# Kernel tuning notes

Measured on AMD Instinct MI355X. Metric: run time of the kernel, lower is better.

Reference implementation:

```python
import jax, jax.numpy as jnp
import numpy as np

N_NODES = 50000
N_EDGES = 800000
IN_DIM = 256     # state_size
HID = 256        # hidden_dim
ACT = 64         # action_size


def gcn_conv(x, src, dst, norm, W, b):
    # PyG GCNConv: out[dst] += norm_e * (x @ W)[src]; then + bias
    h = x @ W                               # [N, out]
    msg = h[src] * norm[:, None]            # [E+N, out]
    agg = jax.ops.segment_sum(msg, dst, num_segments=N_NODES)
    return agg + b


def gcn_norm(edge_index):
    # add self-loops, symmetric normalization deg^-1/2[src]*deg^-1/2[dst]
    loops = jnp.arange(N_NODES, dtype=edge_index.dtype)
    src = jnp.concatenate([edge_index[0], loops])
    dst = jnp.concatenate([edge_index[1], loops])
    deg = jax.ops.segment_sum(jnp.ones_like(dst, dtype=jnp.float32), dst,
                              num_segments=N_NODES)
    dinv = jnp.where(deg > 0, jax.lax.rsqrt(deg), 0.0)
    norm = dinv[src] * dinv[dst]            # [E+N]
    return src, dst, norm


def setup_inputs() -> dict:
    key = jax.random.key(0)
    ks = jax.random.split(key, 12)
    x = jax.random.normal(ks[0], (N_NODES, IN_DIM), dtype=jnp.float32)
    edge_index = jax.random.randint(ks[1], (2, N_EDGES), 0, N_NODES, dtype=jnp.int64)

    def glorot(k, shape):
        lim = float(np.sqrt(6.0 / (shape[0] + shape[1])))
        return jax.random.uniform(k, shape, jnp.float32, -lim, lim)

    return {
        "x": x, "edge_index": edge_index,
        "W1": glorot(ks[2], (IN_DIM, HID)), "b1": jnp.zeros((HID,), jnp.float32),
        "W2": glorot(ks[3], (HID, HID)),    "b2": jnp.zeros((HID,), jnp.float32),
        "fcW1": glorot(ks[4], (HID, HID)),  "fcb1": jnp.zeros((HID,), jnp.float32),
        "fcW2": glorot(ks[5], (HID, HID)),  "fcb2": jnp.zeros((HID,), jnp.float32),
        "fcW3": glorot(ks[6], (HID, ACT)),  "fcb3": jnp.zeros((ACT,), jnp.float32),
    }


def reference(x, edge_index, W1, b1, W2, b2, fcW1, fcb1, fcW2, fcb2, fcW3, fcb3):
    src, dst, norm = gcn_norm(edge_index)
    h = jax.nn.relu(gcn_conv(x, src, dst, norm, W1, b1))   # GNNLayer 1
    h = jax.nn.relu(gcn_conv(h, src, dst, norm, W2, b2))   # GNNLayer 2
    g = jax.nn.relu(jnp.mean(h, axis=0)[None, :])          # [1, HID]
    g = jax.nn.relu(g @ fcW1 + fcb1)
    g = jax.nn.relu(g @ fcW2 + fcb2)
    return g @ fcW3 + fcb3                                 # [1, ACT]
```

## Files before the change

kernel.cpp:

```cpp
#include <hip/hip_runtime.h>

#define N_NODES 50000
#define N_EDGES 800000
#define DIM 256
#define ACT 64
#define SCAN_B 256
#define SCAN_NB ((N_NODES + SCAN_B - 1) / SCAN_B)
#define SLICE_ELEMS ((size_t)N_NODES * 32)
#define AGG_CHUNKS 512
#define NPC ((N_NODES + AGG_CHUNKS - 1) / AGG_CHUNKS)
#define CSR_MAX (N_EDGES + 8 * N_NODES + 64)

typedef __attribute__((ext_vector_type(8))) short short8_t;
typedef __attribute__((ext_vector_type(4))) float f32x4;
typedef __attribute__((ext_vector_type(4))) unsigned short ushort4_t;

__device__ __forceinline__ unsigned short f2b(float x) {
    unsigned u = __float_as_uint(x);
    unsigned r = u + 0x7FFFu + ((u >> 16) & 1u);
    return (unsigned short)(r >> 16);
}


__global__ __launch_bounds__(256) void k_cvt_wt2(const float* __restrict__ W1,
                                                 const float* __restrict__ W2,
                                                 unsigned short* __restrict__ W1t,
                                                 unsigned short* __restrict__ W2t) {
    int b = blockIdx.x;
    const float* W = (b < 256) ? W1 : W2;
    unsigned short* Wt = (b < 256) ? W1t : W2t;
    int i = (b & 255) * 256 + threadIdx.x;
    int k = i >> 8, n = i & 255;
    Wt[n * DIM + k] = f2b(W[k * DIM + n]);
}


__global__ void k_deg_count(const int* __restrict__ ei, int* degi) {
    int e = blockIdx.x * blockDim.x + threadIdx.x;
    if (e < N_EDGES) atomicAdd(&degi[ei[N_EDGES + e]], 1);
}


__global__ __launch_bounds__(SCAN_B) void k_scan_local(const int* __restrict__ degi,
                                                       int* lexc, int* btot) {
    __shared__ int sm[SCAN_B];
    int t = threadIdx.x;
    int i = blockIdx.x * SCAN_B + t;
    int v = (i < N_NODES) ? ((degi[i] + 8) & ~7) : 0;
    sm[t] = v;
    __syncthreads();
#pragma unroll
    for (int off = 1; off < SCAN_B; off <<= 1) {
        int u = (t >= off) ? sm[t - off] : 0;
        __syncthreads();
        sm[t] += u;
        __syncthreads();
    }
    if (i < N_NODES) lexc[i] = sm[t] - v;
    if (t == SCAN_B - 1) btot[blockIdx.x] = sm[t];
}

__global__ __launch_bounds__(SCAN_B) void k_scan_tops(const int* __restrict__ btot,
                                                      int* bbase, int* rowstart) {
    __shared__ int sm[SCAN_B];
    int t = threadIdx.x;
    int v = (t < SCAN_NB) ? btot[t] : 0;
    sm[t] = v;
    __syncthreads();
#pragma unroll
    for (int off = 1; off < SCAN_B; off <<= 1) {
        int u = (t >= off) ? sm[t - off] : 0;
        __syncthreads();
        sm[t] += u;
        __syncthreads();
    }
    if (t < SCAN_NB) bbase[t] = sm[t] - v;
    if (t == SCAN_NB - 1) rowstart[N_NODES] = sm[t];
}

__global__ __launch_bounds__(SCAN_B) void k_scan_apply(const int* __restrict__ degi,
                                                       const int* __restrict__ lexc,
                                                       const int* __restrict__ bbase,
                                                       int* rowstart, int* fillpos,
                                                       float* dinv, unsigned* csr4) {
    int i = blockIdx.x * SCAN_B + threadIdx.x;
    if (i >= N_NODES) return;
    int rs = bbase[blockIdx.x] + lexc[i];
    rowstart[i] = rs;
    int d = degi[i] + 1;
    float di = rsqrtf((float)d);
    dinv[i] = di;
    csr4[rs] = ((unsigned)i << 16) | f2b(di * di);
    fillpos[i] = rs + 1;
}

__global__ void k_fill_edge(const int* __restrict__ ei,
                            const float* __restrict__ dinv, int* fillpos,
                            unsigned* csr4) {
    int e = blockIdx.x * blockDim.x + threadIdx.x;
    if (e < N_EDGES) {
        int s = ei[e];
        int d = ei[N_EDGES + e];
        int p = atomicAdd(&fillpos[d], 1);
        csr4[p] = ((unsigned)s << 16) | f2b(dinv[s] * dinv[d]);
    }
}


template <int AFP32>
__global__ __launch_bounds__(512) void k_gemm_mfma(const void* __restrict__ Ap,
                                                   const unsigned short* __restrict__ Wt,
                                                   unsigned short* __restrict__ H,
                                                   int M) {
    __shared__ char lds[49152];
    char* AsB = lds;
    char* BsB = lds + 16384;

    int tid = threadIdx.x;
    int w = tid >> 6;
    int l = tid & 63;
    int wr = w >> 2, wc = w & 3;
    int r0 = blockIdx.x * 128;

    f32x4 acc[4][4];
#pragma unroll
    for (int i = 0; i < 4; ++i)
#pragma unroll
        for (int j = 0; j < 4; ++j) acc[i][j] = (f32x4)(0.f);

    for (int kt = 0; kt < 4; ++kt) {
        int k0 = kt * 64;
#pragma unroll
        for (int i = 0; i < 2; ++i) {
            int c = tid + i * 512;
            int row = c >> 3, kc = c & 7;
            int gg = r0 + row; if (gg >= M) gg = M - 1;
            short8_t v;
            if (AFP32) {
                const float* A = (const float*)Ap;
                const float4* src = (const float4*)(A + (size_t)gg * DIM + k0 + kc * 8);
                float4 f0 = src[0], f1 = src[1];
                v[0] = (short)f2b(f0.x); v[1] = (short)f2b(f0.y);
                v[2] = (short)f2b(f0.z); v[3] = (short)f2b(f0.w);
                v[4] = (short)f2b(f1.x); v[5] = (short)f2b(f1.y);
                v[6] = (short)f2b(f1.z); v[7] = (short)f2b(f1.w);
            } else {
                const unsigned short* A = (const unsigned short*)Ap;
                int k = k0 + kc * 8;
                int slice = k >> 5, within = k & 31;
                v = *(const short8_t*)(A + (size_t)slice * SLICE_ELEMS + (size_t)gg * 32 + within);
            }
            int off = (row * 128 + kc * 16) ^ ((row & 7) << 4);
            *(short8_t*)(AsB + off) = v;
        }
#pragma unroll
        for (int i = 0; i < 4; ++i) {
            int c = tid + i * 512;
            int n = c >> 3, kc = c & 7;
            short8_t v = *(const short8_t*)(Wt + n * DIM + k0 + kc * 8);
            int off = (n * 128 + kc * 16) ^ ((n & 7) << 4);
            *(short8_t*)(BsB + off) = v;
        }
        __syncthreads();

#pragma unroll
        for (int kf = 0; kf < 2; ++kf) {
            int kb = kf * 64 + (l >> 4) * 16;
            short8_t a[4], b[4];
#pragma unroll
            for (int fm = 0; fm < 4; ++fm) {
                int ra = wr * 64 + fm * 16 + (l & 15);
                a[fm] = *(const short8_t*)(AsB + ((ra * 128 + kb) ^ ((ra & 7) << 4)));
            }
#pragma unroll
            for (int fn = 0; fn < 4; ++fn) {
                int nb = wc * 64 + fn * 16 + (l & 15);
                b[fn] = *(const short8_t*)(BsB + ((nb * 128 + kb) ^ ((nb & 7) << 4)));
            }
#pragma unroll
            for (int fm = 0; fm < 4; ++fm)
#pragma unroll
                for (int fn = 0; fn < 4; ++fn)
                    acc[fm][fn] = __builtin_amdgcn_mfma_f32_16x16x32_bf16(
                        a[fm], b[fn], acc[fm][fn], 0, 0, 0);
        }
        __syncthreads();
    }

#pragma unroll
    for (int fm = 0; fm < 4; ++fm) {
#pragma unroll
        for (int i = 0; i < 4; ++i) {
            int row = r0 + wr * 64 + fm * 16 + ((l >> 4) << 2) + i;
            if (row >= M) continue;
#pragma unroll
            for (int fn = 0; fn < 4; ++fn) {
                int col = wc * 64 + fn * 16 + (l & 15);
                int slice = col >> 5;
                H[(size_t)slice * SLICE_ELEMS + (size_t)row * 32 + (col & 31)] = f2b(acc[fm][fn][i]);
            }
        }
    }
}


__global__ __launch_bounds__(256) void k_agg_sliced(const unsigned short* __restrict__ H,
                                                    const int* __restrict__ rowstart,
                                                    const unsigned* __restrict__ csr4,
                                                    const float* __restrict__ bias,
                                                    unsigned short* __restrict__ X,
                                                    float* __restrict__ gsum,
                                                    int write_out) {
    __shared__ unsigned pbuf[32][2][32];
    int slice = blockIdx.x & 7;
    int chunk = blockIdx.x >> 3;
    int g = threadIdx.x >> 3;
    int lane = threadIdx.x & 7;
    const char* Hb = (const char*)(H + (size_t)slice * SLICE_ELEMS) + (lane << 3);
    unsigned short* Xs = X + (size_t)slice * SLICE_ELEMS;
    int d0 = slice * 32 + lane * 4;
    float4 bb = *(const float4*)&bias[d0];
    float c0 = 0.f, c1 = 0.f, c2 = 0.f, c3 = 0.f;
    int nEnd = (chunk + 1) * NPC; if (nEnd > N_NODES) nEnd = N_NODES;
    for (int n = chunk * NPC + g; n < nEnd; n += 32) {
        int beg = rowstart[n], end = rowstart[n + 1];
        float a0 = 0.f, a1 = 0.f, a2 = 0.f, a3 = 0.f;
        uint4 u = *(const uint4*)(csr4 + beg + (lane << 2));
        int r = 0;
        for (int e = beg; e < end; e += 32, ++r) {
            int en = (e + 32 < end) ? e + 32 : e;
            uint4 un = *(const uint4*)(csr4 + en + (lane << 2));
            unsigned* pb = &pbuf[g][r & 1][0];
            *(uint4*)(pb + (lane << 2)) = u;
#pragma unroll
            for (int s = 0; s < 4; ++s) {
                if (e + (s << 3) >= end) break;
#pragma unroll
                for (int i = 0; i < 8; ++i) {
                    unsigned p = pb[(s << 3) + i];
                    unsigned off = (p >> 16) << 6;
                    float nm = __uint_as_float(p << 16);
                    uint2 q = *(const uint2*)(Hb + off);
                    a0 = fmaf(nm, __uint_as_float(q.x << 16), a0);
                    a1 = fmaf(nm, __uint_as_float(q.x & 0xFFFF0000u), a1);
                    a2 = fmaf(nm, __uint_as_float(q.y << 16), a2);
                    a3 = fmaf(nm, __uint_as_float(q.y & 0xFFFF0000u), a3);
                }
            }
            u = un;
        }
        float o0 = fmaxf(a0 + bb.x, 0.f);
        float o1 = fmaxf(a1 + bb.y, 0.f);
        float o2 = fmaxf(a2 + bb.z, 0.f);
        float o3 = fmaxf(a3 + bb.w, 0.f);
        if (write_out) {
            ushort4_t o; o.x = f2b(o0); o.y = f2b(o1); o.z = f2b(o2); o.w = f2b(o3);
            *(ushort4_t*)(Xs + (size_t)n * 32 + (lane << 2)) = o;
        }
        c0 += o0; c1 += o1; c2 += o2; c3 += o3;
    }
    if (gsum) {
        __shared__ float4 smr[256];
        int tid = threadIdx.x;
        smr[tid] = make_float4(c0, c1, c2, c3);
        __syncthreads();
#pragma unroll
        for (int off = 128; off >= 8; off >>= 1) {
            if (tid < off) {
                float4 a = smr[tid], b = smr[tid + off];
                smr[tid] = make_float4(a.x + b.x, a.y + b.y, a.z + b.z, a.w + b.w);
            }
            __syncthreads();
        }
        if (tid < 8) {
            float4 v = smr[tid];
            atomicAdd(&gsum[d0], v.x);
            atomicAdd(&gsum[d0 + 1], v.y);
            atomicAdd(&gsum[d0 + 2], v.z);
            atomicAdd(&gsum[d0 + 3], v.w);
        }
    }
}


__global__ __launch_bounds__(256) void k_fc(const float* __restrict__ gsum,
                                            const float* __restrict__ fcW1,
                                            const float* __restrict__ fcb1,
                                            const float* __restrict__ fcW2,
                                            const float* __restrict__ fcb2,
                                            const float* __restrict__ fcW3,
                                            const float* __restrict__ fcb3,
                                            float* __restrict__ out) {
    __shared__ float g[DIM];
    __shared__ float h[DIM];
    int t = threadIdx.x;
    g[t] = fmaxf(gsum[t] * (1.0f / (float)N_NODES), 0.f);
    __syncthreads();
    float acc = fcb1[t];
    for (int k = 0; k < DIM; ++k) acc = fmaf(g[k], fcW1[k * DIM + t], acc);
    h[t] = fmaxf(acc, 0.f);
    __syncthreads();
    acc = fcb2[t];
    for (int k = 0; k < DIM; ++k) acc = fmaf(h[k], fcW2[k * DIM + t], acc);
    __syncthreads();
    g[t] = fmaxf(acc, 0.f);
    __syncthreads();
    if (t < ACT) {
        float o = fcb3[t];
        for (int k = 0; k < DIM; ++k) o = fmaf(g[k], fcW3[k * ACT + t], o);
        out[t] = o;
    }
}


extern "C" void kernel_launch(void* const* d_in, const int* in_sizes, int n_in,
                              void* d_out, int out_size, void* d_ws, size_t ws_size,
                              hipStream_t stream) {
    const float* x    = (const float*)d_in[0];
    const int*   ei   = (const int*)d_in[1];
    const float* W1   = (const float*)d_in[2];
    const float* b1   = (const float*)d_in[3];
    const float* W2   = (const float*)d_in[4];
    const float* b2   = (const float*)d_in[5];
    const float* fcW1 = (const float*)d_in[6];
    const float* fcb1 = (const float*)d_in[7];
    const float* fcW2 = (const float*)d_in[8];
    const float* fcb2 = (const float*)d_in[9];
    const float* fcW3 = (const float*)d_in[10];
    const float* fcb3 = (const float*)d_in[11];
    float* out = (float*)d_out;

    char* w = (char*)d_ws;
    size_t o = 0;
#define CARVE(name, type, count) \
    type* name = (type*)(w + o); \
    o += (((size_t)(count) * sizeof(type)) + 255) & ~(size_t)255;
    CARVE(degi, int, N_NODES)
    CARVE(rowstart, int, N_NODES + 1)
    CARVE(fillpos, int, N_NODES)
    CARVE(dinv, float, N_NODES)
    CARVE(lexc, int, N_NODES)
    CARVE(btot, int, SCAN_NB)
    CARVE(bbase, int, SCAN_NB)
    CARVE(csr4, unsigned, CSR_MAX)
    CARVE(gsum, float, DIM)
    CARVE(W1t, unsigned short, DIM * DIM)
    CARVE(W2t, unsigned short, DIM * DIM)
    CARVE(Hbuf, unsigned short, (size_t)N_NODES * DIM)
    CARVE(Xbuf, unsigned short, (size_t)N_NODES * DIM)
#undef CARVE

    hipMemsetAsync(gsum, 0, DIM * sizeof(float), stream);
    hipMemsetAsync(degi, 0, N_NODES * sizeof(int), stream);
    hipMemsetAsync(csr4, 0, (size_t)CSR_MAX * sizeof(unsigned), stream);

    k_cvt_wt2<<<512, 256, 0, stream>>>(W1, W2, W1t, W2t);

    k_deg_count<<<(N_EDGES + 255) / 256, 256, 0, stream>>>(ei, degi);
    k_scan_local<<<SCAN_NB, SCAN_B, 0, stream>>>(degi, lexc, btot);
    k_scan_tops<<<1, SCAN_B, 0, stream>>>(btot, bbase, rowstart);
    k_scan_apply<<<SCAN_NB, SCAN_B, 0, stream>>>(degi, lexc, bbase, rowstart, fillpos,
                                                 dinv, csr4);
    k_fill_edge<<<(N_EDGES + 255) / 256, 256, 0, stream>>>(ei, dinv, fillpos, csr4);

    int gemm_grid = (N_NODES + 127) / 128;
    k_gemm_mfma<1><<<gemm_grid, 512, 0, stream>>>(x, W1t, Hbuf, N_NODES);
    k_agg_sliced<<<8 * AGG_CHUNKS, 256, 0, stream>>>(Hbuf, rowstart, csr4, b1,
                                                     Xbuf, (float*)nullptr, 1);
    k_gemm_mfma<0><<<gemm_grid, 512, 0, stream>>>(Xbuf, W2t, Hbuf, N_NODES);
    k_agg_sliced<<<8 * AGG_CHUNKS, 256, 0, stream>>>(Hbuf, rowstart, csr4, b2,
                                                     Xbuf, gsum, 0);

    k_fc<<<1, 256, 0, stream>>>(gsum, fcW1, fcb1, fcW2, fcb2, fcW3, fcb3, out);
}
```

Measured before the change: 277.5 us.

## Degree-bin nodes into a permutation to balance aggregation across wavefront groups

Adds a histogram and counting-sort pass that groups nodes by their padded edge-round count. The aggregation kernel then walks nodes through this permutation in a grid-strided pattern instead of contiguous chunks, so the 8-lane groups inside a wavefront handle nodes of similar degree. This is meant to cut divergence and load imbalance between groups. In exchange it adds two small kernels with atomics, and it loses locality in the node order of the output writes. The shared staging buffer is also padded to 68 words per group, which may reduce LDS bank conflicts.

```diff
diff --git a/kernel.cpp b/kernel.cpp
--- a/kernel.cpp
+++ b/kernel.cpp
@@ -8,8 +8,9 @@
 #define SCAN_NB ((N_NODES + SCAN_B - 1) / SCAN_B)
 #define SLICE_ELEMS ((size_t)N_NODES * 32)
 #define AGG_CHUNKS 512
-#define NPC ((N_NODES + AGG_CHUNKS - 1) / AGG_CHUNKS)
+#define TOTAL_GROUPS (AGG_CHUNKS * 32)
 #define CSR_MAX (N_EDGES + 8 * N_NODES + 64)
+#define NBINS 16
 
 typedef __attribute__((ext_vector_type(8))) short short8_t;
 typedef __attribute__((ext_vector_type(4))) float f32x4;
@@ -41,6 +42,25 @@
 }
 
 
+__global__ __launch_bounds__(256) void k_hist(const int* __restrict__ degi, int* hist) {
+    int i = blockIdx.x * blockDim.x + threadIdx.x;
+    if (i >= N_NODES) return;
+    int rounds = ((degi[i] + 8) & ~7) >> 3;
+    if (rounds > NBINS - 1) rounds = NBINS - 1;
+    atomicAdd(&hist[rounds], 1);
+}
+
+__global__ __launch_bounds__(256) void k_perm(const int* __restrict__ degi,
+                                              int* histbase, int* perm) {
+    int i = blockIdx.x * blockDim.x + threadIdx.x;
+    if (i >= N_NODES) return;
+    int rounds = ((degi[i] + 8) & ~7) >> 3;
+    if (rounds > NBINS - 1) rounds = NBINS - 1;
+    int pos = atomicAdd(&histbase[rounds], 1);
+    perm[pos] = i;
+}
+
+
 __global__ __launch_bounds__(SCAN_B) void k_scan_local(const int* __restrict__ degi,
                                                        int* lexc, int* btot) {
     __shared__ int sm[SCAN_B];
@@ -61,7 +81,9 @@
 }
 
 __global__ __launch_bounds__(SCAN_B) void k_scan_tops(const int* __restrict__ btot,
-                                                      int* bbase, int* rowstart) {
+                                                      int* bbase, int* rowstart,
+                                                      const int* __restrict__ hist,
+                                                      int* histbase) {
     __shared__ int sm[SCAN_B];
     int t = threadIdx.x;
     int v = (t < SCAN_NB) ? btot[t] : 0;
@@ -76,6 +98,11 @@
     }
     if (t < SCAN_NB) bbase[t] = sm[t] - v;
     if (t == SCAN_NB - 1) rowstart[N_NODES] = sm[t];
+    if (t == 0) {
+        int acc = 0;
+#pragma unroll
+        for (int b = 0; b < NBINS; ++b) { int h = hist[b]; histbase[b] = acc; acc += h; }
+    }
 }
 
 __global__ __launch_bounds__(SCAN_B) void k_scan_apply(const int* __restrict__ degi,
@@ -207,11 +234,12 @@
 __global__ __launch_bounds__(256) void k_agg_sliced(const unsigned short* __restrict__ H,
                                                     const int* __restrict__ rowstart,
                                                     const unsigned* __restrict__ csr4,
+                                                    const int* __restrict__ perm,
                                                     const float* __restrict__ bias,
                                                     unsigned short* __restrict__ X,
                                                     float* __restrict__ gsum,
                                                     int write_out) {
-    __shared__ unsigned pbuf[32][2][32];
+    __shared__ unsigned pbuf[32 * 68];
     int slice = blockIdx.x & 7;
     int chunk = blockIdx.x >> 3;
     int g = threadIdx.x >> 3;
@@ -221,8 +249,10 @@
     int d0 = slice * 32 + lane * 4;
     float4 bb = *(const float4*)&bias[d0];
     float c0 = 0.f, c1 = 0.f, c2 = 0.f, c3 = 0.f;
-    int nEnd = (chunk + 1) * NPC; if (nEnd > N_NODES) nEnd = N_NODES;
-    for (int n = chunk * NPC + g; n < nEnd; n += 32) {
+    unsigned* ps = pbuf + g * 68;
+    int fg = chunk * 32 + g;
+    for (int idx = fg; idx < N_NODES; idx += TOTAL_GROUPS) {
+        int n = perm[idx];
         int beg = rowstart[n], end = rowstart[n + 1];
         float a0 = 0.f, a1 = 0.f, a2 = 0.f, a3 = 0.f;
         uint4 u = *(const uint4*)(csr4 + beg + (lane << 2));
@@ -230,7 +260,7 @@
         for (int e = beg; e < end; e += 32, ++r) {
             int en = (e + 32 < end) ? e + 32 : e;
             uint4 un = *(const uint4*)(csr4 + en + (lane << 2));
-            unsigned* pb = &pbuf[g][r & 1][0];
+            unsigned* pb = ps + (r & 1) * 32;
             *(uint4*)(pb + (lane << 2)) = u;
 #pragma unroll
             for (int s = 0; s < 4; ++s) {
@@ -342,6 +372,9 @@
     CARVE(lexc, int, N_NODES)
     CARVE(btot, int, SCAN_NB)
     CARVE(bbase, int, SCAN_NB)
+    CARVE(hist, int, NBINS)
+    CARVE(histbase, int, NBINS)
+    CARVE(perm, int, N_NODES)
     CARVE(csr4, unsigned, CSR_MAX)
     CARVE(gsum, float, DIM)
     CARVE(W1t, unsigned short, DIM * DIM)
@@ -352,23 +385,26 @@
 
     hipMemsetAsync(gsum, 0, DIM * sizeof(float), stream);
     hipMemsetAsync(degi, 0, N_NODES * sizeof(int), stream);
+    hipMemsetAsync(hist, 0, NBINS * sizeof(int), stream);
     hipMemsetAsync(csr4, 0, (size_t)CSR_MAX * sizeof(unsigned), stream);
 
     k_cvt_wt2<<<512, 256, 0, stream>>>(W1, W2, W1t, W2t);
 
     k_deg_count<<<(N_EDGES + 255) / 256, 256, 0, stream>>>(ei, degi);
+    k_hist<<<SCAN_NB, 256, 0, stream>>>(degi, hist);
     k_scan_local<<<SCAN_NB, SCAN_B, 0, stream>>>(degi, lexc, btot);
-    k_scan_tops<<<1, SCAN_B, 0, stream>>>(btot, bbase, rowstart);
+    k_scan_tops<<<1, SCAN_B, 0, stream>>>(btot, bbase, rowstart, hist, histbase);
+    k_perm<<<SCAN_NB, 256, 0, stream>>>(degi, histbase, perm);
     k_scan_apply<<<SCAN_NB, SCAN_B, 0, stream>>>(degi, lexc, bbase, rowstart, fillpos,
                                                  dinv, csr4);
     k_fill_edge<<<(N_EDGES + 255) / 256, 256, 0, stream>>>(ei, dinv, fillpos, csr4);
 
     int gemm_grid = (N_NODES + 127) / 128;
     k_gemm_mfma<1><<<gemm_grid, 512, 0, stream>>>(x, W1t, Hbuf, N_NODES);
-    k_agg_sliced<<<8 * AGG_CHUNKS, 256, 0, stream>>>(Hbuf, rowstart, csr4, b1,
+    k_agg_sliced<<<8 * AGG_CHUNKS, 256, 0, stream>>>(Hbuf, rowstart, csr4, perm, b1,
                                                      Xbuf, (float*)nullptr, 1);
     k_gemm_mfma<0><<<gemm_grid, 512, 0, stream>>>(Xbuf, W2t, Hbuf, N_NODES);
-    k_agg_sliced<<<8 * AGG_CHUNKS, 256, 0, stream>>>(Hbuf, rowstart, csr4, b2,
+    k_agg_sliced<<<8 * AGG_CHUNKS, 256, 0, stream>>>(Hbuf, rowstart, csr4, perm, b2,
                                                      Xbuf, gsum, 0);
 
     k_fc<<<1, 256, 0, stream>>>(gsum, fcW1, fcb1, fcW2, fcb2, fcW3, fcb3, out);
```

Measured after the change: 1.026 ms. 270% more time.

## Sort nodes into degree bins to balance aggregation work across wavefront groups

Applied to the files above, without the earlier changes.

Adds a counting-sort pass (per-block histogram, scan over bins, permutation scatter) that orders nodes by rounded in-degree. The aggregation kernel then walks nodes through this permutation, strided across all groups, instead of contiguous chunks. Each 8-lane group and each wavefront therefore sees similar edge counts, which cuts tail imbalance and divergence in the edge loop. The cost is three extra small kernels, an indirect perm lookup, and less locality in rowstart and output writes. The shared buffer is also padded to 68 words per group to reduce bank conflicts.

```diff
diff --git a/kernel.cpp b/kernel.cpp
--- a/kernel.cpp
+++ b/kernel.cpp
@@ -8,8 +8,10 @@
 #define SCAN_NB ((N_NODES + SCAN_B - 1) / SCAN_B)
 #define SLICE_ELEMS ((size_t)N_NODES * 32)
 #define AGG_CHUNKS 512
-#define NPC ((N_NODES + AGG_CHUNKS - 1) / AGG_CHUNKS)
+#define TOTAL_GROUPS (AGG_CHUNKS * 32)
 #define CSR_MAX (N_EDGES + 8 * N_NODES + 64)
+#define NBINS 16
+#define NBB (NBINS * SCAN_NB)
 
 typedef __attribute__((ext_vector_type(8))) short short8_t;
 typedef __attribute__((ext_vector_type(4))) float f32x4;
@@ -19,6 +21,11 @@
     unsigned u = __float_as_uint(x);
     unsigned r = u + 0x7FFFu + ((u >> 16) & 1u);
     return (unsigned short)(r >> 16);
+}
+
+__device__ __forceinline__ int deg_bin(int deg) {
+    int rounds = ((deg + 8) & ~7) >> 3;
+    return (rounds > NBINS - 1) ? NBINS - 1 : rounds;
 }
 
 
@@ -38,6 +45,55 @@
 __global__ void k_deg_count(const int* __restrict__ ei, int* degi) {
     int e = blockIdx.x * blockDim.x + threadIdx.x;
     if (e < N_EDGES) atomicAdd(&degi[ei[N_EDGES + e]], 1);
+}
+
+
+__global__ __launch_bounds__(256) void k_hist_rank(const int* __restrict__ degi,
+                                                   int* blockbin,
+                                                   unsigned char* lrank) {
+    __shared__ int lh[NBINS];
+    int t = threadIdx.x;
+    if (t < NBINS) lh[t] = 0;
+    __syncthreads();
+    int i = blockIdx.x * 256 + t;
+    if (i < N_NODES) {
+        int bin = deg_bin(degi[i]);
+        lrank[i] = (unsigned char)atomicAdd(&lh[bin], 1);
+    }
+    __syncthreads();
+    if (t < NBINS) blockbin[t * SCAN_NB + blockIdx.x] = lh[t];
+}
+
+__global__ __launch_bounds__(256) void k_scan_bins(const int* __restrict__ blockbin,
+                                                   int* blockbase) {
+    __shared__ int sm[256];
+    int t = threadIdx.x;
+    const int CH = (NBB + 255) / 256;
+    int s0 = t * CH;
+    int s1 = s0 + CH; if (s1 > NBB) s1 = NBB;
+    int s = 0;
+    for (int i = s0; i < s1; ++i) s += blockbin[i];
+    sm[t] = s;
+    __syncthreads();
+#pragma unroll
+    for (int off = 1; off < 256; off <<= 1) {
+        int u = (t >= off) ? sm[t - off] : 0;
+        __syncthreads();
+        sm[t] += u;
+        __syncthreads();
+    }
+    int base = sm[t] - s;
+    for (int i = s0; i < s1; ++i) { int v = blockbin[i]; blockbase[i] = base; base += v; }
+}
+
+__global__ __launch_bounds__(256) void k_perm_apply(const int* __restrict__ degi,
+                                                    const int* __restrict__ blockbase,
+                                                    const unsigned char* __restrict__ lrank,
+                                                    int* perm) {
+    int i = blockIdx.x * 256 + threadIdx.x;
+    if (i >= N_NODES) return;
+    int bin = deg_bin(degi[i]);
+    perm[blockbase[bin * SCAN_NB + blockIdx.x] + lrank[i]] = i;
 }
 
 
@@ -207,11 +263,12 @@
 __global__ __launch_bounds__(256) void k_agg_sliced(const unsigned short* __restrict__ H,
                                                     const int* __restrict__ rowstart,
                                                     const unsigned* __restrict__ csr4,
+                                                    const int* __restrict__ perm,
                                                     const float* __restrict__ bias,
                                                     unsigned short* __restrict__ X,
                                                     float* __restrict__ gsum,
                                                     int write_out) {
-    __shared__ unsigned pbuf[32][2][32];
+    __shared__ unsigned pbuf[32 * 68];
     int slice = blockIdx.x & 7;
     int chunk = blockIdx.x >> 3;
     int g = threadIdx.x >> 3;
@@ -221,8 +278,10 @@
     int d0 = slice * 32 + lane * 4;
     float4 bb = *(const float4*)&bias[d0];
     float c0 = 0.f, c1 = 0.f, c2 = 0.f, c3 = 0.f;
-    int nEnd = (chunk + 1) * NPC; if (nEnd > N_NODES) nEnd = N_NODES;
-    for (int n = chunk * NPC + g; n < nEnd; n += 32) {
+    unsigned* ps = pbuf + g * 68;
+    int fg = chunk * 32 + g;
+    for (int idx = fg; idx < N_NODES; idx += TOTAL_GROUPS) {
+        int n = perm[idx];
         int beg = rowstart[n], end = rowstart[n + 1];
         float a0 = 0.f, a1 = 0.f, a2 = 0.f, a3 = 0.f;
         uint4 u = *(const uint4*)(csr4 + beg + (lane << 2));
@@ -230,7 +289,7 @@
         for (int e = beg; e < end; e += 32, ++r) {
             int en = (e + 32 < end) ? e + 32 : e;
             uint4 un = *(const uint4*)(csr4 + en + (lane << 2));
-            unsigned* pb = &pbuf[g][r & 1][0];
+            unsigned* pb = ps + (r & 1) * 32;
             *(uint4*)(pb + (lane << 2)) = u;
 #pragma unroll
             for (int s = 0; s < 4; ++s) {
@@ -342,6 +401,10 @@
     CARVE(lexc, int, N_NODES)
     CARVE(btot, int, SCAN_NB)
     CARVE(bbase, int, SCAN_NB)
+    CARVE(blockbin, int, NBB)
+    CARVE(blockbase, int, NBB)
+    CARVE(perm, int, N_NODES)
+    CARVE(lrank, unsigned char, N_NODES)
     CARVE(csr4, unsigned, CSR_MAX)
     CARVE(gsum, float, DIM)
     CARVE(W1t, unsigned short, DIM * DIM)
@@ -357,6 +420,9 @@
     k_cvt_wt2<<<512, 256, 0, stream>>>(W1, W2, W1t, W2t);
 
     k_deg_count<<<(N_EDGES + 255) / 256, 256, 0, stream>>>(ei, degi);
+    k_hist_rank<<<SCAN_NB, 256, 0, stream>>>(degi, blockbin, lrank);
+    k_scan_bins<<<1, 256, 0, stream>>>(blockbin, blockbase);
+    k_perm_apply<<<SCAN_NB, 256, 0, stream>>>(degi, blockbase, lrank, perm);
     k_scan_local<<<SCAN_NB, SCAN_B, 0, stream>>>(degi, lexc, btot);
     k_scan_tops<<<1, SCAN_B, 0, stream>>>(btot, bbase, rowstart);
     k_scan_apply<<<SCAN_NB, SCAN_B, 0, stream>>>(degi, lexc, bbase, rowstart, fillpos,
@@ -365,10 +431,10 @@
 
     int gemm_grid = (N_NODES + 127) / 128;
     k_gemm_mfma<1><<<gemm_grid, 512, 0, stream>>>(x, W1t, Hbuf, N_NODES);
-    k_agg_sliced<<<8 * AGG_CHUNKS, 256, 0, stream>>>(Hbuf, rowstart, csr4, b1,
+    k_agg_sliced<<<8 * AGG_CHUNKS, 256, 0, stream>>>(Hbuf, rowstart, csr4, perm, b1,
                                                      Xbuf, (float*)nullptr, 1);
     k_gemm_mfma<0><<<gemm_grid, 512, 0, stream>>>(Xbuf, W2t, Hbuf, N_NODES);
-    k_agg_sliced<<<8 * AGG_CHUNKS, 256, 0, stream>>>(Hbuf, rowstart, csr4, b2,
+    k_agg_sliced<<<8 * AGG_CHUNKS, 256, 0, stream>>>(Hbuf, rowstart, csr4, perm, b2,
                                                      Xbuf, gsum, 0);
 
     k_fc<<<1, 256, 0, stream>>>(gsum, fcW1, fcb1, fcW2, fcb2, fcW3, fcb3, out);
```

Result: no change. 281.5 us (+1.4%).
